# Optimization experiments

Hardware: AMD Instinct MI355X
Metric: run time of the kernel (lower is better)

Reference implementation:

```python
import jax, jax.numpy as jnp
import numpy as np

GAMMA = 0.99
CLIP_VALUE = 5.0
B, T = 4096, 4096


def setup_inputs() -> dict:
    key = jax.random.key(0)
    k1, k2, k3, k4 = jax.random.split(key, 4)
    return {
        "log_probs": jax.random.normal(k1, (B, T), dtype=jnp.float32),
        "logits": jax.random.normal(k2, (B, T), dtype=jnp.float32),
        "weight": jax.random.uniform(k3, (B, T), dtype=jnp.float32),
        "baselines": jax.random.normal(k4, (B, T), dtype=jnp.float32),
    }


def _discounted_reverse_cumsum(wr):
    # wr: [B, T]. c[t] = wr[t] + GAMMA * c[t+1]  (reverse linear recurrence)
    def step(carry, x):
        c = x + GAMMA * carry
        return c, c
    # scan over time, reversed; xs shape [T, B]
    _, cs = jax.lax.scan(step, jnp.zeros(wr.shape[0], wr.dtype), wr.T, reverse=True)
    return cs.T  # [B, T]


def reference(log_probs, logits, weight, baselines):
    rewards = jax.nn.log_sigmoid(logits)                    # [B, T]
    cumulative_rewards = _discounted_reverse_cumsum(weight * rewards)
    advantages = cumulative_rewards - baselines
    advantages = advantages - advantages.mean(axis=0)       # center over batch
    advantages = jnp.clip(advantages, -CLIP_VALUE, CLIP_VALUE)
    generator_objective = (advantages * log_probs).sum(axis=1)  # [B]
    return generator_objective, cumulative_rewards
```

## Files before the change

### kernel.cpp

```cpp
#include <hip/hip_runtime.h>
#include <math.h>

#define B_DIM 4096
#define T_DIM 4096

constexpr float GAMMA_F = 0.99f;
constexpr float CLIP_V  = 5.0f;

constexpr float G2    = GAMMA_F * GAMMA_F;
constexpr float G4    = G2 * G2;
constexpr float G8    = G4 * G4;
constexpr float Q1    = G8 * G8;
constexpr float Q2    = Q1 * Q1;
constexpr float Q4    = Q2 * Q2;
constexpr float Q8    = Q4 * Q4;
constexpr float Q16   = Q8 * Q8;
constexpr float Q32   = Q16 * Q16;
constexpr float G1024 = Q32 * Q32;

__device__ __forceinline__ float pow_g16(int e) {
    float f = 1.0f;
    if (e & 1)  f *= Q1;
    if (e & 2)  f *= Q2;
    if (e & 4)  f *= Q4;
    if (e & 8)  f *= Q8;
    if (e & 16) f *= Q16;
    if (e & 32) f *= Q32;
    return f;
}

__global__ __launch_bounds__(256) void k_scan(const float* __restrict__ logits,
                                              const float* __restrict__ weight,
                                              float* __restrict__ cum) {
    __shared__ float buf[4352];
    __shared__ float waveS[4];

    const int row = blockIdx.x;
    const int tid = threadIdx.x;
    const size_t base = (size_t)row * T_DIM;

    #pragma unroll
    for (int j = 0; j < 16; ++j) {
        int idx = j * 256 + tid;
        float x = logits[base + idx];
        float w = weight[base + idx];
        float ls = fminf(x, 0.0f) - log1pf(__expf(-fabsf(x)));
        buf[idx + (idx >> 4)] = w * ls;
    }
    __syncthreads();

    float wr[16];
    const int pbase = tid * 17;
    #pragma unroll
    for (int j = 0; j < 16; ++j) wr[j] = buf[pbase + j];
    float V = 0.0f;
    #pragma unroll
    for (int j = 15; j >= 0; --j) V = fmaf(GAMMA_F, V, wr[j]);

    const int wv = tid >> 6, ln = tid & 63;
    float s = V;
    {
        const float F[6] = {Q1, Q2, Q4, Q8, Q16, Q32};
        #pragma unroll
        for (int k = 0; k < 6; ++k) {
            int off = 1 << k;
            float t = __shfl_down(s, off, 64);
            if (ln + off < 64) s = fmaf(F[k], t, s);
        }
    }
    if (ln == 0) waveS[wv] = s;
    __syncthreads();

    float Anext = 0.0f;
    for (int w2 = 3; w2 > wv; --w2) Anext = fmaf(G1024, Anext, waveS[w2]);

    float snext = __shfl_down(s, 1, 64);
    if (ln == 63) snext = 0.0f;
    float carry = fmaf(pow_g16(63 - ln), Anext, snext);

    #pragma unroll
    for (int j = 15; j >= 0; --j) {
        carry = fmaf(GAMMA_F, carry, wr[j]);
        buf[pbase + j] = carry;
    }
    __syncthreads();

    #pragma unroll
    for (int j = 0; j < 16; ++j) {
        int idx = j * 256 + tid;
        cum[base + idx] = buf[idx + (idx >> 4)];
    }
}

__global__ __launch_bounds__(256) void k_colpart(const float* __restrict__ cum,
                                                 const float* __restrict__ baselines,
                                                 float* __restrict__ partials) {
    const int t = blockIdx.x * 256 + threadIdx.x;
    const int r0 = blockIdx.y * 128;
    float sum = 0.0f;
    size_t p = (size_t)r0 * T_DIM + t;
    for (int r = 0; r < 128; ++r, p += T_DIM)
        sum += cum[p] - baselines[p];
    partials[blockIdx.y * T_DIM + t] = sum;
}

__global__ __launch_bounds__(256) void k_colmean(const float* __restrict__ partials,
                                                 float* __restrict__ colmean) {
    const int t = blockIdx.x * 256 + threadIdx.x;
    float s = 0.0f;
    #pragma unroll
    for (int c = 0; c < 32; ++c) s += partials[c * T_DIM + t];
    colmean[t] = s * (1.0f / B_DIM);
}

__global__ __launch_bounds__(256) void k_obj(const float* __restrict__ cum,
                                             const float* __restrict__ baselines,
                                             const float* __restrict__ logp,
                                             const float* __restrict__ colmean,
                                             float* __restrict__ obj) {
    const int row = blockIdx.x, tid = threadIdx.x;
    const size_t base = (size_t)row * T_DIM;
    float acc = 0.0f;
    #pragma unroll
    for (int j = 0; j < 16; ++j) {
        int t = j * 256 + tid;
        float adv = cum[base + t] - baselines[base + t] - colmean[t];
        adv = fminf(fmaxf(adv, -CLIP_V), CLIP_V);
        acc = fmaf(adv, logp[base + t], acc);
    }
    #pragma unroll
    for (int off = 32; off > 0; off >>= 1) acc += __shfl_down(acc, off, 64);
    __shared__ float ws4[4];
    if ((tid & 63) == 0) ws4[tid >> 6] = acc;
    __syncthreads();
    if (tid == 0) obj[row] = (ws4[0] + ws4[1]) + (ws4[2] + ws4[3]);
}

extern "C" void kernel_launch(void* const* d_in, const int* in_sizes, int n_in,
                              void* d_out, int out_size, void* d_ws, size_t ws_size,
                              hipStream_t stream) {
    const float* log_probs = (const float*)d_in[0];
    const float* logits    = (const float*)d_in[1];
    const float* weight    = (const float*)d_in[2];
    const float* baselines = (const float*)d_in[3];

    float* obj = (float*)d_out;
    float* cum = obj + B_DIM;

    float* partials = (float*)d_ws;
    float* colmean  = partials + 32 * T_DIM;

    k_scan   <<<B_DIM,                 256, 0, stream>>>(logits, weight, cum);
    k_colpart<<<dim3(T_DIM / 256, 32), 256, 0, stream>>>(cum, baselines, partials);
    k_colmean<<<T_DIM / 256,           256, 0, stream>>>(partials, colmean);
    k_obj    <<<B_DIM,                 256, 0, stream>>>(cum, baselines, log_probs, colmean, obj);
}
```

Measured before the change: 286.7 us.

## Vectorize scan and objective with float4, merge column reduction via atomics

```diff
diff --git a/kernel.cpp b/kernel.cpp
--- a/kernel.cpp
+++ b/kernel.cpp
@@ -29,30 +29,29 @@
     return f;
 }
 
-__global__ __launch_bounds__(256) void k_scan(const float* __restrict__ logits,
-                                              const float* __restrict__ weight,
-                                              float* __restrict__ cum) {
-    __shared__ float buf[4352];
+__device__ __forceinline__ float lsig(float x) {
+    return fminf(x, 0.0f) - __logf(1.0f + __expf(-fabsf(x)));
+}
+
+__global__ __launch_bounds__(256) void k_scan(const float4* __restrict__ logits,
+                                              const float4* __restrict__ weight,
+                                              float4* __restrict__ cum) {
     __shared__ float waveS[4];
-
     const int row = blockIdx.x;
     const int tid = threadIdx.x;
-    const size_t base = (size_t)row * T_DIM;
-
-    #pragma unroll
-    for (int j = 0; j < 16; ++j) {
-        int idx = j * 256 + tid;
-        float x = logits[base + idx];
-        float w = weight[base + idx];
-        float ls = fminf(x, 0.0f) - log1pf(__expf(-fabsf(x)));
-        buf[idx + (idx >> 4)] = w * ls;
-    }
-    __syncthreads();
+    const size_t base4 = (size_t)row * (T_DIM / 4) + (size_t)tid * 4;
 
     float wr[16];
-    const int pbase = tid * 17;
     #pragma unroll
-    for (int j = 0; j < 16; ++j) wr[j] = buf[pbase + j];
+    for (int k = 0; k < 4; ++k) {
+        float4 x4 = logits[base4 + k];
+        float4 w4 = weight[base4 + k];
+        wr[4 * k + 0] = w4.x * lsig(x4.x);
+        wr[4 * k + 1] = w4.y * lsig(x4.y);
+        wr[4 * k + 2] = w4.z * lsig(x4.z);
+        wr[4 * k + 3] = w4.w * lsig(x4.w);
+    }
+
     float V = 0.0f;
     #pragma unroll
     for (int j = 15; j >= 0; --j) V = fmaf(GAMMA_F, V, wr[j]);
@@ -79,54 +78,60 @@
     float carry = fmaf(pow_g16(63 - ln), Anext, snext);
 
     #pragma unroll
-    for (int j = 15; j >= 0; --j) {
-        carry = fmaf(GAMMA_F, carry, wr[j]);
-        buf[pbase + j] = carry;
-    }
-    __syncthreads();
-
-    #pragma unroll
-    for (int j = 0; j < 16; ++j) {
-        int idx = j * 256 + tid;
-        cum[base + idx] = buf[idx + (idx >> 4)];
+    for (int k = 3; k >= 0; --k) {
+        float4 o4;
+        o4.w = carry = fmaf(GAMMA_F, carry, wr[4 * k + 3]);
+        o4.z = carry = fmaf(GAMMA_F, carry, wr[4 * k + 2]);
+        o4.y = carry = fmaf(GAMMA_F, carry, wr[4 * k + 1]);
+        o4.x = carry = fmaf(GAMMA_F, carry, wr[4 * k + 0]);
+        cum[base4 + k] = o4;
     }
 }
 
-__global__ __launch_bounds__(256) void k_colpart(const float* __restrict__ cum,
-                                                 const float* __restrict__ baselines,
-                                                 float* __restrict__ partials) {
-    const int t = blockIdx.x * 256 + threadIdx.x;
-    const int r0 = blockIdx.y * 128;
-    float sum = 0.0f;
-    size_t p = (size_t)r0 * T_DIM + t;
-    for (int r = 0; r < 128; ++r, p += T_DIM)
-        sum += cum[p] - baselines[p];
-    partials[blockIdx.y * T_DIM + t] = sum;
+__global__ __launch_bounds__(256) void k_zero(float* __restrict__ p) {
+    p[blockIdx.x * 256 + threadIdx.x] = 0.0f;
 }
 
-__global__ __launch_bounds__(256) void k_colmean(const float* __restrict__ partials,
-                                                 float* __restrict__ colmean) {
+__global__ __launch_bounds__(256) void k_colsum(const float* __restrict__ cum,
+                                                const float* __restrict__ baselines,
+                                                float* __restrict__ colsum) {
     const int t = blockIdx.x * 256 + threadIdx.x;
-    float s = 0.0f;
+    size_t p = (size_t)(blockIdx.y * 32) * T_DIM + t;
+    float s0 = 0.0f, s1 = 0.0f, s2 = 0.0f, s3 = 0.0f;
     #pragma unroll
-    for (int c = 0; c < 32; ++c) s += partials[c * T_DIM + t];
-    colmean[t] = s * (1.0f / B_DIM);
+    for (int r = 0; r < 32; r += 4) {
+        s0 += cum[p] - baselines[p];               p += T_DIM;
+        s1 += cum[p] - baselines[p];               p += T_DIM;
+        s2 += cum[p] - baselines[p];               p += T_DIM;
+        s3 += cum[p] - baselines[p];               p += T_DIM;
+    }
+    atomicAdd(&colsum[t], (s0 + s1) + (s2 + s3));
 }
 
-__global__ __launch_bounds__(256) void k_obj(const float* __restrict__ cum,
-                                             const float* __restrict__ baselines,
-                                             const float* __restrict__ logp,
-                                             const float* __restrict__ colmean,
+__global__ __launch_bounds__(256) void k_obj(const float4* __restrict__ cum,
+                                             const float4* __restrict__ baselines,
+                                             const float4* __restrict__ logp,
+                                             const float4* __restrict__ colsum,
                                              float* __restrict__ obj) {
+    constexpr float invB = 1.0f / B_DIM;
     const int row = blockIdx.x, tid = threadIdx.x;
-    const size_t base = (size_t)row * T_DIM;
+    const size_t base4 = (size_t)row * (T_DIM / 4);
     float acc = 0.0f;
     #pragma unroll
-    for (int j = 0; j < 16; ++j) {
-        int t = j * 256 + tid;
-        float adv = cum[base + t] - baselines[base + t] - colmean[t];
-        adv = fminf(fmaxf(adv, -CLIP_V), CLIP_V);
-        acc = fmaf(adv, logp[base + t], acc);
+    for (int j = 0; j < 4; ++j) {
+        int t4 = j * 256 + tid;
+        float4 c = cum[base4 + t4];
+        float4 b = baselines[base4 + t4];
+        float4 l = logp[base4 + t4];
+        float4 m = colsum[t4];
+        float a0 = fminf(fmaxf(c.x - b.x - m.x * invB, -CLIP_V), CLIP_V);
+        float a1 = fminf(fmaxf(c.y - b.y - m.y * invB, -CLIP_V), CLIP_V);
+        float a2 = fminf(fmaxf(c.z - b.z - m.z * invB, -CLIP_V), CLIP_V);
+        float a3 = fminf(fmaxf(c.w - b.w - m.w * invB, -CLIP_V), CLIP_V);
+        acc = fmaf(a0, l.x, acc);
+        acc = fmaf(a1, l.y, acc);
+        acc = fmaf(a2, l.z, acc);
+        acc = fmaf(a3, l.w, acc);
     }
     #pragma unroll
     for (int off = 32; off > 0; off >>= 1) acc += __shfl_down(acc, off, 64);
@@ -146,12 +151,12 @@
 
     float* obj = (float*)d_out;
     float* cum = obj + B_DIM;
+    float* colsum = (float*)d_ws;
 
-    float* partials = (float*)d_ws;
-    float* colmean  = partials + 32 * T_DIM;
-
-    k_scan   <<<B_DIM,                 256, 0, stream>>>(logits, weight, cum);
-    k_colpart<<<dim3(T_DIM / 256, 32), 256, 0, stream>>>(cum, baselines, partials);
-    k_colmean<<<T_DIM / 256,           256, 0, stream>>>(partials, colmean);
-    k_obj    <<<B_DIM,                 256, 0, stream>>>(cum, baselines, log_probs, colmean, obj);
+    k_zero  <<<T_DIM / 256, 256, 0, stream>>>(colsum);
+    k_scan  <<<B_DIM, 256, 0, stream>>>((const float4*)logits, (const float4*)weight,
+                                        (float4*)cum);
+    k_colsum<<<dim3(T_DIM / 256, 128), 256, 0, stream>>>(cum, baselines, colsum);
+    k_obj   <<<B_DIM, 256, 0, stream>>>((const float4*)cum, (const float4*)baselines,
+                                        (const float4*)log_probs, (const float4*)colsum, obj);
 }
```

New measurement: 279.1 us. 2.7% less time.
